# Optimization experiments

Hardware: AMD Instinct MI355X
Metric: run time of the kernel (lower is better)

## Reference

```python
import jax, jax.numpy as jnp
import numpy as np

N_QUBITS = 10
N_LAYERS = 3


def _apply_1q(state, gate, q, batched):
    # state: (B,) + (2,)*n ; gate: (2,2) or (B,2,2)
    s = jnp.moveaxis(state, q + 1, -1)
    shp = s.shape
    s = s.reshape(shp[0], -1, 2)
    eq = 'bij,brj->bri' if batched else 'ij,brj->bri'
    s = jnp.einsum(eq, gate, s).reshape(shp)
    return jnp.moveaxis(s, -1, q + 1)


def _apply_cnot(state, c, t):
    s = jnp.moveaxis(state, (c + 1, t + 1), (-2, -1))
    s = s.at[..., 1, :].set(s[..., 1, ::-1])  # flip target where control==1
    return jnp.moveaxis(s, (-2, -1), (c + 1, t + 1))


def _rot_gate(phi, theta, omega):
    # PennyLane Rot(phi,theta,omega) = RZ(omega) @ RY(theta) @ RZ(phi)
    ch = jnp.cos(theta * 0.5).astype(jnp.complex64)
    sh = jnp.sin(theta * 0.5).astype(jnp.complex64)
    m00 = jnp.exp(-1j * (phi + omega) * 0.5) * ch
    m01 = -jnp.exp(1j * (phi - omega) * 0.5) * sh
    m10 = jnp.exp(-1j * (phi - omega) * 0.5) * sh
    m11 = jnp.exp(1j * (phi + omega) * 0.5) * ch
    return jnp.stack([jnp.stack([m00, m01]), jnp.stack([m10, m11])])


def _circuit(x, weights):
    B = x.shape[0]
    n = N_QUBITS
    state = jnp.zeros((B,) + (2,) * n, jnp.complex64)
    state = state.at[(slice(None),) + (0,) * n].set(1.0)  # |0...0>
    c = jnp.cos(x * 0.5)  # (B, n)
    s = jnp.sin(x * 0.5)
    for l in range(N_LAYERS):
        # AngleEmbedding: RY(x_q) on each wire (batched gates)
        for q in range(n):
            g = jnp.stack([jnp.stack([c[:, q], -s[:, q]], -1),
                           jnp.stack([s[:, q], c[:, q]], -1)], -2).astype(jnp.complex64)
            state = _apply_1q(state, g, q, True)
        # StronglyEntanglingLayers, single sub-layer: Rot on each wire
        for q in range(n):
            g = _rot_gate(weights[l, q, 0], weights[l, q, 1], weights[l, q, 2])
            state = _apply_1q(state, g, q, False)
        # ring of CNOTs with range r=1
        for q in range(n):
            state = _apply_cnot(state, q, (q + 1) % n)
    probs = jnp.abs(state) ** 2  # (B,) + (2,)*n, real
    outs = []
    for q in range(n):
        axes = tuple(a for a in range(1, n + 1) if a != q + 1)
        m = probs.sum(axis=axes)  # (B, 2)
        outs.append(m[:, 0] - m[:, 1])  # <Z_q>
    return jnp.stack(outs, axis=1).astype(jnp.float32)


def setup_inputs() -> dict:
    key = jax.random.key(0)
    k1, k2 = jax.random.split(key)
    x = jax.random.normal(k1, (4096, N_QUBITS), dtype=jnp.float32)
    weights = jax.random.uniform(k2, (N_LAYERS, N_QUBITS, 3), dtype=jnp.float32,
                                 minval=-np.pi, maxval=np.pi)
    return {"x": x, "weights": weights}


def reference(x, weights):
    return _circuit(x, weights)
```

## Files before the change

### kernel.cpp

```cpp
#include <hip/hip_runtime.h>

#define NQ 10
#define NL 3

typedef float v2f __attribute__((ext_vector_type(2)));

__device__ __forceinline__ int   f2i(float v) { union { float f; int i; } u; u.f = v; return u.i; }
__device__ __forceinline__ float i2f(int v)   { union { int i; float f; } u; u.i = v; return u.f; }

__device__ __forceinline__ v2f cmul(v2f a, v2f b) {
    v2f d;
    asm("v_pk_mul_f32 %0, %1, %2 op_sel:[0,0] op_sel_hi:[0,1]"
        : "=v"(d) : "v"(a), "v"(b));
    asm("v_pk_fma_f32 %0, %1, %2, %0 op_sel:[1,1,0] op_sel_hi:[1,0,1] neg_lo:[0,1,0]"
        : "+v"(d) : "v"(a), "v"(b));
    return d;
}

__device__ __forceinline__ v2f pk_ab(v2f A, v2f B, v2f cs) {
    v2f d;
    asm("v_pk_mul_f32 %0, %1, %2 op_sel:[0,1] op_sel_hi:[1,1]"
        : "=v"(d) : "v"(B), "v"(cs));
    asm("v_pk_fma_f32 %0, %1, %2, %0 op_sel:[0,0,0] op_sel_hi:[1,0,1]"
        : "+v"(d) : "v"(A), "v"(cs));
    return d;
}
__device__ __forceinline__ v2f pk_ab_n(v2f A, v2f B, v2f cs) {
    v2f d;
    asm("v_pk_mul_f32 %0, %1, %2 op_sel:[0,1] op_sel_hi:[1,1] neg_lo:[1,0] neg_hi:[1,0]"
        : "=v"(d) : "v"(B), "v"(cs));
    asm("v_pk_fma_f32 %0, %1, %2, %0 op_sel:[0,0,0] op_sel_hi:[1,0,1]"
        : "+v"(d) : "v"(A), "v"(cs));
    return d;
}

template<int C> __device__ __forceinline__ int dppm(int v) {
    return __builtin_amdgcn_mov_dpp(v, C, 0xF, 0xF, false);
}

template<int LM>
__device__ __forceinline__ v2f xlane(v2f v, int baddr) {
    if constexpr (LM == 0) return v;
    int x = f2i(v.x), y = f2i(v.y);
    if constexpr (LM == 1)       { x = dppm<177>(x); y = dppm<177>(y); }
    else if constexpr (LM == 2)  { x = dppm<78>(x);  y = dppm<78>(y); }
    else if constexpr (LM == 3)  { x = dppm<27>(x);  y = dppm<27>(y); }
    else if constexpr (LM < 32) {
        constexpr int off = (LM << 10) | 0x1F;
        x = __builtin_amdgcn_ds_swizzle(x, off);
        y = __builtin_amdgcn_ds_swizzle(y, off);
    } else {
        x = __builtin_amdgcn_ds_bpermute(baddr, x);
        y = __builtin_amdgcn_ds_bpermute(baddr, y);
    }
    return (v2f){ i2f(x), i2f(y) };
}

template<int MASK, int RMASK>
__device__ __forceinline__ void apply_gate(v2f (&a)[16], float4 r0, float4 r1,
                                           float cq, float sq, int lane)
{
    constexpr int LM = (MASK >> 4) & 63;
    constexpr int JM = MASK & 15;
    constexpr int RH = (RMASK >> 4) & 63;
    constexpr int RL = RMASK & 15;

    const v2f vcs = { cq, sq };
    const v2f r0a = { r0.x, r0.y }, r0b = { r0.z, r0.w };
    const v2f r1a = { r1.x, r1.y }, r1b = { r1.z, r1.w };
    const v2f g00 = pk_ab  (r0a, r0b, vcs);
    const v2f g01 = pk_ab_n(r0b, r0a, vcs);
    const v2f g10 = pk_ab  (r1a, r1b, vcs);
    const v2f g11 = pk_ab_n(r1b, r1a, vcs);

    const bool lp = (RH != 0) && (__popc(lane & RH) & 1);
    const v2f A0 = lp ? g11 : g00;
    const v2f B0 = lp ? g10 : g01;
    const v2f A1 = lp ? g00 : g11;
    const v2f B1 = lp ? g01 : g10;

    const int baddr = ((lane ^ LM) << 2);

    v2f o[16];
    #pragma unroll
    for (int j = 0; j < 16; ++j) o[j] = xlane<LM>(a[j ^ JM], baddr);

#define QNN_F(J) { constexpr int SP_ = __builtin_popcount((J) & RL) & 1;      \
    const v2f CA = SP_ ? A1 : A0;                                             \
    const v2f CB = SP_ ? B1 : B0;                                             \
    const v2f av = a[J]; const v2f ov = o[J];                                 \
    v2f d;                                                                    \
    asm("v_pk_mul_f32 %0, %1, %2 op_sel:[0,0] op_sel_hi:[0,1]"                \
        : "=v"(d) : "v"(CA), "v"(av));                    \
    asm("v_pk_fma_f32 %0, %1, %2, %0 op_sel:[1,1,0] op_sel_hi:[1,0,1] neg_lo:[0,1,0]" \
        : "+v"(d) : "v"(CA), "v"(av));                  \
    asm("v_pk_fma_f32 %0, %1, %2, %0 op_sel:[0,0,0] op_sel_hi:[0,1,1]"        \
        : "+v"(d) : "v"(CB), "v"(ov));                  \
    asm("v_pk_fma_f32 %0, %1, %2, %0 op_sel:[1,1,0] op_sel_hi:[1,0,1] neg_lo:[0,1,0]" \
        : "+v"(d) : "v"(CB), "v"(ov));                  \
    a[J] = d; }
    QNN_F(0) QNN_F(1) QNN_F(2) QNN_F(3) QNN_F(4) QNN_F(5) QNN_F(6) QNN_F(7)
    QNN_F(8) QNN_F(9) QNN_F(10) QNN_F(11) QNN_F(12) QNN_F(13) QNN_F(14) QNN_F(15)
#undef QNN_F
}

__global__ __launch_bounds__(256, 4)
void qnn_kernel(const float* __restrict__ x, const float* __restrict__ w,
                float* __restrict__ out)
{
    __shared__ float4 rotL[NL * NQ][2];

    const int t    = threadIdx.x;
    const int lane = t & 63;
    const int b    = blockIdx.x * 4 + (t >> 6);

    if (t < NL * NQ) {
        const float* wp = w + t * 3;
        float phi = wp[0], th = wp[1], om = wp[2];
        float ct = cosf(th * 0.5f), st = sinf(th * 0.5f);
        float ap = (phi + om) * 0.5f, am = (phi - om) * 0.5f;
        float cap = cosf(ap), sap = sinf(ap);
        float cam = cosf(am), sam = sinf(am);
        rotL[t][0] = make_float4(cap * ct, -sap * ct, -cam * st, -sam * st);
        rotL[t][1] = make_float4(cam * st, -sam * st,  cap * ct,  sap * ct);
    }
    __syncthreads();

    const float* xb = x + (size_t)__builtin_amdgcn_readfirstlane(b * NQ);
    float c_[NQ], s_[NQ];
    #pragma unroll
    for (int q = 0; q < NQ; ++q) {
        float xv = xb[q] * 0.5f;
        c_[q] = i2f(__builtin_amdgcn_readfirstlane(f2i(__cosf(xv))));
        s_[q] = i2f(__builtin_amdgcn_readfirstlane(f2i(__sinf(xv))));
    }

    v2f c0[4], c1[4];
    v2f Ln = {1.f, 0.f};
    #pragma unroll
    for (int q = 0; q < NQ; ++q) {
        float4 r0 = rotL[q][0], r1 = rotL[q][1];
        const v2f vcs = { c_[q], s_[q] };
        const v2f r0a = { r0.x, r0.y }, r0b = { r0.z, r0.w };
        const v2f r1a = { r1.x, r1.y }, r1b = { r1.z, r1.w };
        v2f g0 = pk_ab(r0a, r0b, vcs);
        v2f g1 = pk_ab(r1a, r1b, vcs);
        if (q < 4) { c0[q] = g0; c1[q] = g1; }
        else {
            v2f gg = ((lane >> (q - 4)) & 1) ? g1 : g0;
            Ln = (q == 4) ? gg : cmul(Ln, gg);
        }
    }
    v2f S01[4], SH[4];
    #pragma unroll
    for (int j = 0; j < 4; ++j)
        S01[j] = cmul((j & 1) ? c1[0] : c0[0], (j & 2) ? c1[1] : c0[1]);
    #pragma unroll
    for (int h = 0; h < 4; ++h)
        SH[h] = cmul(cmul((h & 1) ? c1[2] : c0[2], (h & 2) ? c1[3] : c0[3]), Ln);
    v2f a[16];
    #pragma unroll
    for (int j = 0; j < 16; ++j)
        a[j] = cmul(S01[j & 3], SH[j >> 2]);

#define GATE(IDX, Q, MASK, RMASK) \
    apply_gate<MASK, RMASK>(a, rotL[IDX][0], rotL[IDX][1], c_[Q], s_[Q], lane);
    GATE(10, 0, 0x003, 0x3FE)  GATE(11, 1, 0x006, 0x003)
    GATE(12, 2, 0x00C, 0x007)  GATE(13, 3, 0x018, 0x00F)
    GATE(14, 4, 0x030, 0x01F)  GATE(15, 5, 0x060, 0x03F)
    GATE(16, 6, 0x0C0, 0x07F)  GATE(17, 7, 0x180, 0x0FF)
    GATE(18, 8, 0x300, 0x1FF)  GATE(19, 9, 0x203, 0x3FF)
    GATE(20, 0, 0x005, 0x2AB)  GATE(21, 1, 0x00A, 0x3FD)
    GATE(22, 2, 0x014, 0x3FA)  GATE(23, 3, 0x028, 0x3F5)
    GATE(24, 4, 0x050, 0x3EA)  GATE(25, 5, 0x0A0, 0x3D5)
    GATE(26, 6, 0x140, 0x3AA)  GATE(27, 7, 0x280, 0x355)
    GATE(28, 8, 0x103, 0x2AA)  GATE(29, 9, 0x206, 0x155)
#undef GATE

    float P[16];
    #pragma unroll
    for (int j = 0; j < 16; ++j)
        P[j] = fmaf(a[j].x, a[j].x, a[j].y * a[j].y);
    #pragma unroll
    for (int bit = 0; bit < 4; ++bit) {
        #pragma unroll
        for (int j = 0; j < 16; ++j)
            if (!(j & (1 << bit))) {
                int k = j | (1 << bit);
                float u = P[j], v = P[k];
                P[j] = u + v;
                P[k] = u - v;
            }
    }

    const int bp32 = ((lane ^ 32) << 2);
    float vout = 0.f;
#define MEAS(Q, RM)                                                           \
    { constexpr int RH_ = ((RM) >> 4) & 63;                                   \
      constexpr int RL_ = (RM) & 15;                                          \
      float v = P[RL_];                                                       \
      if (__popc(lane & RH_) & 1) v = -v;                                     \
      v += i2f(dppm<177>(f2i(v)));                                 \
      v += i2f(dppm<78>(f2i(v)));                                  \
      v += i2f(dppm<321>(dppm<27>(f2i(v))));                  \
      v += i2f(dppm<320>(dppm<321>(f2i(v))));                \
      v += i2f(__builtin_amdgcn_ds_swizzle(f2i(v), (16 << 10) | 0x1F));       \
      v += i2f(__builtin_amdgcn_ds_bpermute(bp32, f2i(v)));                   \
      if (lane == (Q)) vout = v; }
    MEAS(0, 0x0CD) MEAS(1, 0x156) MEAS(2, 0x2AC) MEAS(3, 0x159)
    MEAS(4, 0x2B3) MEAS(5, 0x166) MEAS(6, 0x2CC) MEAS(7, 0x199)
    MEAS(8, 0x333) MEAS(9, 0x266)
#undef MEAS

    if (lane < NQ) out[b * NQ + lane] = vout;
}

extern "C" void kernel_launch(void* const* d_in, const int* in_sizes, int n_in,
                              void* d_out, int out_size, void* d_ws, size_t ws_size,
                              hipStream_t stream) {
    const float* x = (const float*)d_in[0];
    const float* w = (const float*)d_in[1];
    float* out = (float*)d_out;
    const int B = in_sizes[0] / NQ;
    qnn_kernel<<<B / 4, 256, 0, stream>>>(x, w, out);
}
```

Measured before the change: 75.52 us.

## Process two batch samples per wavefront and use permlane swaps for reductions

```diff
diff --git a/kernel.cpp b/kernel.cpp
--- a/kernel.cpp
+++ b/kernel.cpp
@@ -4,6 +4,7 @@
 #define NL 3
 
 typedef float v2f __attribute__((ext_vector_type(2)));
+typedef unsigned int u2 __attribute__((ext_vector_type(2)));
 
 __device__ __forceinline__ int   f2i(float v) { union { float f; int i; } u; u.f = v; return u.i; }
 __device__ __forceinline__ float i2f(int v)   { union { int i; float f; } u; u.i = v; return u.f; }
@@ -36,6 +37,17 @@
 
 template<int C> __device__ __forceinline__ int dppm(int v) {
     return __builtin_amdgcn_mov_dpp(v, C, 0xF, 0xF, false);
+}
+
+__device__ __forceinline__ void pl16_pair(int &x, int &y) {
+    u2 r1 = __builtin_amdgcn_permlane16_swap((unsigned)x, (unsigned)y, false, false);
+    u2 r2 = __builtin_amdgcn_permlane16_swap(r1[1], r1[0], false, false);
+    x = (int)r2[0]; y = (int)r2[1];
+}
+__device__ __forceinline__ void pl32_pair(int &x, int &y) {
+    u2 r1 = __builtin_amdgcn_permlane32_swap((unsigned)x, (unsigned)y, false, false);
+    u2 r2 = __builtin_amdgcn_permlane32_swap(r1[1], r1[0], false, false);
+    x = (int)r2[0]; y = (int)r2[1];
 }
 
 template<int LM>
@@ -57,38 +69,55 @@
 }
 
 template<int MASK, int RMASK>
-__device__ __forceinline__ void apply_gate(v2f (&a)[16], float4 r0, float4 r1,
-                                           float cq, float sq, int lane)
+__device__ __forceinline__ void apply_gate2(v2f (&a0)[16], v2f (&a1)[16],
+                                            float4 r0, float4 r1,
+                                            float cqA, float sqA,
+                                            float cqB, float sqB, int lane)
 {
     constexpr int LM = (MASK >> 4) & 63;
     constexpr int JM = MASK & 15;
     constexpr int RH = (RMASK >> 4) & 63;
     constexpr int RL = RMASK & 15;
 
-    const v2f vcs = { cq, sq };
+    const int baddr = ((lane ^ LM) << 2);
+
+    v2f o0[16];
+    #pragma unroll
+    for (int j = 0; j < 16; ++j) o0[j] = xlane<LM>(a0[j ^ JM], baddr);
+
     const v2f r0a = { r0.x, r0.y }, r0b = { r0.z, r0.w };
     const v2f r1a = { r1.x, r1.y }, r1b = { r1.z, r1.w };
-    const v2f g00 = pk_ab  (r0a, r0b, vcs);
-    const v2f g01 = pk_ab_n(r0b, r0a, vcs);
-    const v2f g10 = pk_ab  (r1a, r1b, vcs);
-    const v2f g11 = pk_ab_n(r1b, r1a, vcs);
-
     const bool lp = (RH != 0) && (__popc(lane & RH) & 1);
-    const v2f A0 = lp ? g11 : g00;
-    const v2f B0 = lp ? g10 : g01;
-    const v2f A1 = lp ? g00 : g11;
-    const v2f B1 = lp ? g01 : g10;
-
-    const int baddr = ((lane ^ LM) << 2);
-
-    v2f o[16];
-    #pragma unroll
-    for (int j = 0; j < 16; ++j) o[j] = xlane<LM>(a[j ^ JM], baddr);
-
-#define QNN_F(J) { constexpr int SP_ = __builtin_popcount((J) & RL) & 1;      \
-    const v2f CA = SP_ ? A1 : A0;                                             \
-    const v2f CB = SP_ ? B1 : B0;                                             \
-    const v2f av = a[J]; const v2f ov = o[J];                                 \
+
+    const v2f vcsA = { cqA, sqA };
+    const v2f g00A = pk_ab  (r0a, r0b, vcsA);
+    const v2f g01A = pk_ab_n(r0b, r0a, vcsA);
+    const v2f g10A = pk_ab  (r1a, r1b, vcsA);
+    const v2f g11A = pk_ab_n(r1b, r1a, vcsA);
+    const v2f A0A = lp ? g11A : g00A;
+    const v2f B0A = lp ? g10A : g01A;
+    const v2f A1A = lp ? g00A : g11A;
+    const v2f B1A = lp ? g01A : g10A;
+
+    const v2f vcsB = { cqB, sqB };
+    const v2f g00B = pk_ab  (r0a, r0b, vcsB);
+    const v2f g01B = pk_ab_n(r0b, r0a, vcsB);
+    const v2f g10B = pk_ab  (r1a, r1b, vcsB);
+    const v2f g11B = pk_ab_n(r1b, r1a, vcsB);
+    const v2f A0B = lp ? g11B : g00B;
+    const v2f B0B = lp ? g10B : g01B;
+    const v2f A1B = lp ? g00B : g11B;
+    const v2f B1B = lp ? g01B : g10B;
+
+    v2f o1[16];
+    #pragma unroll
+    for (int j = 0; j < 16; ++j) o1[j] = xlane<LM>(a1[j ^ JM], baddr);
+
+#define QNN_F(ARR, OARR, A0_, A1_, B0_, B1_, J) {                             \
+    constexpr int SP_ = __builtin_popcount((J) & RL) & 1;                     \
+    const v2f CA = SP_ ? A1_ : A0_;                                           \
+    const v2f CB = SP_ ? B1_ : B0_;                                           \
+    const v2f av = ARR[J]; const v2f ov = OARR[J];                            \
     v2f d;                                                                    \
     asm("v_pk_mul_f32 %0, %1, %2 op_sel:[0,0] op_sel_hi:[0,1]"                \
         : "=v"(d) : "v"(CA), "v"(av));                    \
@@ -98,48 +127,32 @@
         : "+v"(d) : "v"(CB), "v"(ov));                  \
     asm("v_pk_fma_f32 %0, %1, %2, %0 op_sel:[1,1,0] op_sel_hi:[1,0,1] neg_lo:[0,1,0]" \
         : "+v"(d) : "v"(CB), "v"(ov));                  \
-    a[J] = d; }
-    QNN_F(0) QNN_F(1) QNN_F(2) QNN_F(3) QNN_F(4) QNN_F(5) QNN_F(6) QNN_F(7)
-    QNN_F(8) QNN_F(9) QNN_F(10) QNN_F(11) QNN_F(12) QNN_F(13) QNN_F(14) QNN_F(15)
+    ARR[J] = d; }
+#define FMA16(ARR, OARR, A0_, A1_, B0_, B1_)                                  \
+    QNN_F(ARR,OARR,A0_,A1_,B0_,B1_,0)  QNN_F(ARR,OARR,A0_,A1_,B0_,B1_,1)      \
+    QNN_F(ARR,OARR,A0_,A1_,B0_,B1_,2)  QNN_F(ARR,OARR,A0_,A1_,B0_,B1_,3)      \
+    QNN_F(ARR,OARR,A0_,A1_,B0_,B1_,4)  QNN_F(ARR,OARR,A0_,A1_,B0_,B1_,5)      \
+    QNN_F(ARR,OARR,A0_,A1_,B0_,B1_,6)  QNN_F(ARR,OARR,A0_,A1_,B0_,B1_,7)      \
+    QNN_F(ARR,OARR,A0_,A1_,B0_,B1_,8)  QNN_F(ARR,OARR,A0_,A1_,B0_,B1_,9)      \
+    QNN_F(ARR,OARR,A0_,A1_,B0_,B1_,10) QNN_F(ARR,OARR,A0_,A1_,B0_,B1_,11)     \
+    QNN_F(ARR,OARR,A0_,A1_,B0_,B1_,12) QNN_F(ARR,OARR,A0_,A1_,B0_,B1_,13)     \
+    QNN_F(ARR,OARR,A0_,A1_,B0_,B1_,14) QNN_F(ARR,OARR,A0_,A1_,B0_,B1_,15)
+
+    FMA16(a0, o0, A0A, A1A, B0A, B1A)
+    FMA16(a1, o1, A0B, A1B, B0B, B1B)
+#undef FMA16
 #undef QNN_F
 }
 
-__global__ __launch_bounds__(256, 4)
-void qnn_kernel(const float* __restrict__ x, const float* __restrict__ w,
-                float* __restrict__ out)
+__device__ __forceinline__ void layer1(v2f (&a)[16], const float (&c_)[NQ],
+                                       const float (&s_)[NQ],
+                                       const float4 (*rot)[2], int lane)
 {
-    __shared__ float4 rotL[NL * NQ][2];
-
-    const int t    = threadIdx.x;
-    const int lane = t & 63;
-    const int b    = blockIdx.x * 4 + (t >> 6);
-
-    if (t < NL * NQ) {
-        const float* wp = w + t * 3;
-        float phi = wp[0], th = wp[1], om = wp[2];
-        float ct = cosf(th * 0.5f), st = sinf(th * 0.5f);
-        float ap = (phi + om) * 0.5f, am = (phi - om) * 0.5f;
-        float cap = cosf(ap), sap = sinf(ap);
-        float cam = cosf(am), sam = sinf(am);
-        rotL[t][0] = make_float4(cap * ct, -sap * ct, -cam * st, -sam * st);
-        rotL[t][1] = make_float4(cam * st, -sam * st,  cap * ct,  sap * ct);
-    }
-    __syncthreads();
-
-    const float* xb = x + (size_t)__builtin_amdgcn_readfirstlane(b * NQ);
-    float c_[NQ], s_[NQ];
-    #pragma unroll
-    for (int q = 0; q < NQ; ++q) {
-        float xv = xb[q] * 0.5f;
-        c_[q] = i2f(__builtin_amdgcn_readfirstlane(f2i(__cosf(xv))));
-        s_[q] = i2f(__builtin_amdgcn_readfirstlane(f2i(__sinf(xv))));
-    }
-
     v2f c0[4], c1[4];
     v2f Ln = {1.f, 0.f};
     #pragma unroll
     for (int q = 0; q < NQ; ++q) {
-        float4 r0 = rotL[q][0], r1 = rotL[q][1];
+        float4 r0 = rot[q][0], r1 = rot[q][1];
         const v2f vcs = { c_[q], s_[q] };
         const v2f r0a = { r0.x, r0.y }, r0b = { r0.z, r0.w };
         const v2f r1a = { r1.x, r1.y }, r1b = { r1.z, r1.w };
@@ -158,13 +171,52 @@
     #pragma unroll
     for (int h = 0; h < 4; ++h)
         SH[h] = cmul(cmul((h & 1) ? c1[2] : c0[2], (h & 2) ? c1[3] : c0[3]), Ln);
-    v2f a[16];
     #pragma unroll
     for (int j = 0; j < 16; ++j)
         a[j] = cmul(S01[j & 3], SH[j >> 2]);
-
-#define GATE(IDX, Q, MASK, RMASK) \
-    apply_gate<MASK, RMASK>(a, rotL[IDX][0], rotL[IDX][1], c_[Q], s_[Q], lane);
+}
+
+__global__ __launch_bounds__(256, 2)
+void qnn_kernel(const float* __restrict__ x, const float* __restrict__ w,
+                float* __restrict__ out)
+{
+    __shared__ float4 rotL[NL * NQ][2];
+
+    const int t    = threadIdx.x;
+    const int lane = t & 63;
+    const int wv   = blockIdx.x * 4 + (t >> 6);
+
+    if (t < NL * NQ) {
+        const float* wp = w + t * 3;
+        float phi = wp[0], th = wp[1], om = wp[2];
+        float ct = cosf(th * 0.5f), st = sinf(th * 0.5f);
+        float ap = (phi + om) * 0.5f, am = (phi - om) * 0.5f;
+        float cap = cosf(ap), sap = sinf(ap);
+        float cam = cosf(am), sam = sinf(am);
+        rotL[t][0] = make_float4(cap * ct, -sap * ct, -cam * st, -sam * st);
+        rotL[t][1] = make_float4(cam * st, -sam * st,  cap * ct,  sap * ct);
+    }
+    __syncthreads();
+
+    const float* xb = x + (size_t)__builtin_amdgcn_readfirstlane(wv * 2 * NQ);
+    float cA[NQ], sA[NQ], cB[NQ], sB[NQ];
+    #pragma unroll
+    for (int q = 0; q < NQ; ++q) {
+        float xv = xb[q] * 0.5f;
+        cA[q] = i2f(__builtin_amdgcn_readfirstlane(f2i(__cosf(xv))));
+        sA[q] = i2f(__builtin_amdgcn_readfirstlane(f2i(__sinf(xv))));
+        float xw = xb[NQ + q] * 0.5f;
+        cB[q] = i2f(__builtin_amdgcn_readfirstlane(f2i(__cosf(xw))));
+        sB[q] = i2f(__builtin_amdgcn_readfirstlane(f2i(__sinf(xw))));
+    }
+
+    v2f a0[16], a1[16];
+    layer1(a0, cA, sA, rotL, lane);
+    layer1(a1, cB, sB, rotL, lane);
+
+#define GATE(IDX, Q, MASK, RMASK)                                             \
+    apply_gate2<MASK, RMASK>(a0, a1, rotL[IDX][0], rotL[IDX][1],              \
+                             cA[Q], sA[Q], cB[Q], sB[Q], lane);
     GATE(10, 0, 0x003, 0x3FE)  GATE(11, 1, 0x006, 0x003)
     GATE(12, 2, 0x00C, 0x007)  GATE(13, 3, 0x018, 0x00F)
     GATE(14, 4, 0x030, 0x01F)  GATE(15, 5, 0x060, 0x03F)
@@ -177,42 +229,56 @@
     GATE(28, 8, 0x103, 0x2AA)  GATE(29, 9, 0x206, 0x155)
 #undef GATE
 
-    float P[16];
+    v2f P[16];
     #pragma unroll
     for (int j = 0; j < 16; ++j)
-        P[j] = fmaf(a[j].x, a[j].x, a[j].y * a[j].y);
+        P[j] = (v2f){ fmaf(a0[j].x, a0[j].x, a0[j].y * a0[j].y),
+                      fmaf(a1[j].x, a1[j].x, a1[j].y * a1[j].y) };
     #pragma unroll
     for (int bit = 0; bit < 4; ++bit) {
         #pragma unroll
         for (int j = 0; j < 16; ++j)
             if (!(j & (1 << bit))) {
                 int k = j | (1 << bit);
-                float u = P[j], v = P[k];
+                v2f u = P[j], v = P[k];
                 P[j] = u + v;
                 P[k] = u - v;
             }
     }
 
-    const int bp32 = ((lane ^ 32) << 2);
-    float vout = 0.f;
+    v2f vout = {0.f, 0.f};
 #define MEAS(Q, RM)                                                           \
     { constexpr int RH_ = ((RM) >> 4) & 63;                                   \
       constexpr int RL_ = (RM) & 15;                                          \
-      float v = P[RL_];                                                       \
+      v2f v = P[RL_];                                                         \
       if (__popc(lane & RH_) & 1) v = -v;                                     \
-      v += i2f(dppm<177>(f2i(v)));                                 \
-      v += i2f(dppm<78>(f2i(v)));                                  \
-      v += i2f(dppm<321>(dppm<27>(f2i(v))));                  \
-      v += i2f(dppm<320>(dppm<321>(f2i(v))));                \
-      v += i2f(__builtin_amdgcn_ds_swizzle(f2i(v), (16 << 10) | 0x1F));       \
-      v += i2f(__builtin_amdgcn_ds_bpermute(bp32, f2i(v)));                   \
+      v2f tt;                                                                 \
+      tt.x = i2f(dppm<177>(f2i(v.x))); tt.y = i2f(dppm<177>(f2i(v.y)));       \
+      v += tt;                                                     \
+      tt.x = i2f(dppm<78>(f2i(v.x)));  tt.y = i2f(dppm<78>(f2i(v.y)));        \
+      v += tt;                                                     \
+      tt.x = i2f(dppm<321>(dppm<27>(f2i(v.x))));                              \
+      tt.y = i2f(dppm<321>(dppm<27>(f2i(v.y))));                              \
+      v += tt;                                                \
+      tt.x = i2f(dppm<320>(dppm<321>(f2i(v.x))));                             \
+      tt.y = i2f(dppm<320>(dppm<321>(f2i(v.y))));                             \
+      v += tt;                                               \
+      { int px = f2i(v.x), py = f2i(v.y); pl16_pair(px, py);                  \
+        tt = (v2f){ i2f(px), i2f(py) }; }                                     \
+      v += tt;                                        \
+      { int px = f2i(v.x), py = f2i(v.y); pl32_pair(px, py);                  \
+        tt = (v2f){ i2f(px), i2f(py) }; }                                     \
+      v += tt;                                        \
       if (lane == (Q)) vout = v; }
     MEAS(0, 0x0CD) MEAS(1, 0x156) MEAS(2, 0x2AC) MEAS(3, 0x159)
     MEAS(4, 0x2B3) MEAS(5, 0x166) MEAS(6, 0x2CC) MEAS(7, 0x199)
     MEAS(8, 0x333) MEAS(9, 0x266)
 #undef MEAS
 
-    if (lane < NQ) out[b * NQ + lane] = vout;
+    if (lane < NQ) {
+        out[(wv * 2)     * NQ + lane] = vout.x;
+        out[(wv * 2 + 1) * NQ + lane] = vout.y;
+    }
 }
 
 extern "C" void kernel_launch(void* const* d_in, const int* in_sizes, int n_in,
@@ -222,5 +288,5 @@
     const float* w = (const float*)d_in[1];
     float* out = (float*)d_out;
     const int B = in_sizes[0] / NQ;
-    qnn_kernel<<<B / 4, 256, 0, stream>>>(x, w, out);
-}
+    qnn_kernel<<<B / 8, 256, 0, stream>>>(x, w, out);
+}
```

New measurement: 77.35 us. 1.02x slower.

## Split each state vector across two wavefronts with LDS exchange for bit-3 gates

Applied to the files above, without the earlier changes.

```diff
diff --git a/kernel.cpp b/kernel.cpp
--- a/kernel.cpp
+++ b/kernel.cpp
@@ -7,6 +7,9 @@
 
 __device__ __forceinline__ int   f2i(float v) { union { float f; int i; } u; u.f = v; return u.i; }
 __device__ __forceinline__ float i2f(int v)   { union { int i; float f; } u; u.i = v; return u.f; }
+__device__ __forceinline__ float uf(float v) {
+    return i2f(__builtin_amdgcn_readfirstlane(f2i(v)));
+}
 
 __device__ __forceinline__ v2f cmul(v2f a, v2f b) {
     v2f d;
@@ -16,7 +19,6 @@
         : "+v"(d) : "v"(a), "v"(b));
     return d;
 }
-
 __device__ __forceinline__ v2f pk_ab(v2f A, v2f B, v2f cs) {
     v2f d;
     asm("v_pk_mul_f32 %0, %1, %2 op_sel:[0,1] op_sel_hi:[1,1]"
@@ -56,14 +58,32 @@
     return (v2f){ i2f(x), i2f(y) };
 }
 
-template<int MASK, int RMASK>
-__device__ __forceinline__ void apply_gate(v2f (&a)[16], float4 r0, float4 r1,
-                                           float cq, float sq, int lane)
+template<int MASK, int RMASK, bool CROSS>
+__device__ __forceinline__ void agate(v2f (&a)[8], float4 r0, float4 r1,
+                                      float cq, float sq, int lane, int wid,
+                                      v2f (*xch)[8][64])
 {
-    constexpr int LM = (MASK >> 4) & 63;
-    constexpr int JM = MASK & 15;
-    constexpr int RH = (RMASK >> 4) & 63;
-    constexpr int RL = RMASK & 15;
+    constexpr int LM  = (MASK >> 4) & 63;
+    constexpr int JM  = MASK & 15;
+    constexpr int JML = JM & 7;
+    constexpr int RH  = (RMASK >> 4) & 63;
+    constexpr int RL  = RMASK & 15;
+    constexpr int RL3 = (RL >> 3) & 1;
+    constexpr int RLL = RL & 7;
+
+    v2f o[8];
+    if constexpr (!CROSS) {
+        const int baddr = ((lane ^ LM) << 2);
+        #pragma unroll
+        for (int j = 0; j < 8; ++j) o[j] = xlane<LM>(a[j ^ JML], baddr);
+    } else {
+        #pragma unroll
+        for (int j = 0; j < 8; ++j) xch[wid][j][lane] = a[j];
+        __syncthreads();
+        #pragma unroll
+        for (int j = 0; j < 8; ++j) o[j] = xch[wid ^ 1][j ^ JML][lane ^ LM];
+        __syncthreads();
+    }
 
     const v2f vcs = { cq, sq };
     const v2f r0a = { r0.x, r0.y }, r0b = { r0.z, r0.w };
@@ -73,19 +93,14 @@
     const v2f g10 = pk_ab  (r1a, r1b, vcs);
     const v2f g11 = pk_ab_n(r1b, r1a, vcs);
 
-    const bool lp = (RH != 0) && (__popc(lane & RH) & 1);
-    const v2f A0 = lp ? g11 : g00;
-    const v2f B0 = lp ? g10 : g01;
-    const v2f A1 = lp ? g00 : g11;
-    const v2f B1 = lp ? g01 : g10;
-
-    const int baddr = ((lane ^ LM) << 2);
-
-    v2f o[16];
-    #pragma unroll
-    for (int j = 0; j < 16; ++j) o[j] = xlane<LM>(a[j ^ JM], baddr);
-
-#define QNN_F(J) { constexpr int SP_ = __builtin_popcount((J) & RL) & 1;      \
+    const bool lp0 = (RH != 0) && (__popc(lane & RH) & 1);
+    const bool lpw = lp0 != ((RL3 != 0) && (wid != 0));
+    const v2f A0 = lpw ? g11 : g00;
+    const v2f B0 = lpw ? g10 : g01;
+    const v2f A1 = lpw ? g00 : g11;
+    const v2f B1 = lpw ? g01 : g10;
+
+#define QNN_F(J) { constexpr int SP_ = __builtin_popcount((J) & RLL) & 1;     \
     const v2f CA = SP_ ? A1 : A0;                                             \
     const v2f CB = SP_ ? B1 : B0;                                             \
     const v2f av = a[J]; const v2f ov = o[J];                                 \
@@ -100,19 +115,20 @@
         : "+v"(d) : "v"(CB), "v"(ov));                  \
     a[J] = d; }
     QNN_F(0) QNN_F(1) QNN_F(2) QNN_F(3) QNN_F(4) QNN_F(5) QNN_F(6) QNN_F(7)
-    QNN_F(8) QNN_F(9) QNN_F(10) QNN_F(11) QNN_F(12) QNN_F(13) QNN_F(14) QNN_F(15)
 #undef QNN_F
 }
 
-__global__ __launch_bounds__(256, 4)
+__global__ __launch_bounds__(128, 8)
 void qnn_kernel(const float* __restrict__ x, const float* __restrict__ w,
                 float* __restrict__ out)
 {
     __shared__ float4 rotL[NL * NQ][2];
+    __shared__ v2f    xch[2][8][64];
 
     const int t    = threadIdx.x;
     const int lane = t & 63;
-    const int b    = blockIdx.x * 4 + (t >> 6);
+    const int wid  = t >> 6;
+    const int b    = blockIdx.x;
 
     if (t < NL * NQ) {
         const float* wp = w + t * 3;
@@ -126,13 +142,13 @@
     }
     __syncthreads();
 
-    const float* xb = x + (size_t)__builtin_amdgcn_readfirstlane(b * NQ);
+    const float* xb = x + (size_t)b * NQ;
     float c_[NQ], s_[NQ];
     #pragma unroll
     for (int q = 0; q < NQ; ++q) {
         float xv = xb[q] * 0.5f;
-        c_[q] = i2f(__builtin_amdgcn_readfirstlane(f2i(__cosf(xv))));
-        s_[q] = i2f(__builtin_amdgcn_readfirstlane(f2i(__sinf(xv))));
+        c_[q] = uf(__cosf(xv));
+        s_[q] = uf(__sinf(xv));
     }
 
     v2f c0[4], c1[4];
@@ -158,13 +174,14 @@
     #pragma unroll
     for (int h = 0; h < 4; ++h)
         SH[h] = cmul(cmul((h & 1) ? c1[2] : c0[2], (h & 2) ? c1[3] : c0[3]), Ln);
-    v2f a[16];
-    #pragma unroll
-    for (int j = 0; j < 16; ++j)
-        a[j] = cmul(S01[j & 3], SH[j >> 2]);
-
-#define GATE(IDX, Q, MASK, RMASK) \
-    apply_gate<MASK, RMASK>(a, rotL[IDX][0], rotL[IDX][1], c_[Q], s_[Q], lane);
+    v2f a[8];
+    #pragma unroll
+    for (int j = 0; j < 8; ++j)
+        a[j] = cmul(S01[j & 3], SH[(wid << 1) | (j >> 2)]);
+
+#define GATE(IDX, Q, MASK, RMASK)                                             \
+    agate<MASK, RMASK, ((MASK & 8) != 0)>(a, rotL[IDX][0], rotL[IDX][1],      \
+                                          c_[Q], s_[Q], lane, wid, xch);
     GATE(10, 0, 0x003, 0x3FE)  GATE(11, 1, 0x006, 0x003)
     GATE(12, 2, 0x00C, 0x007)  GATE(13, 3, 0x018, 0x00F)
     GATE(14, 4, 0x030, 0x01F)  GATE(15, 5, 0x060, 0x03F)
@@ -177,14 +194,14 @@
     GATE(28, 8, 0x103, 0x2AA)  GATE(29, 9, 0x206, 0x155)
 #undef GATE
 
-    float P[16];
-    #pragma unroll
-    for (int j = 0; j < 16; ++j)
+    float P[8];
+    #pragma unroll
+    for (int j = 0; j < 8; ++j)
         P[j] = fmaf(a[j].x, a[j].x, a[j].y * a[j].y);
     #pragma unroll
-    for (int bit = 0; bit < 4; ++bit) {
-        #pragma unroll
-        for (int j = 0; j < 16; ++j)
+    for (int bit = 0; bit < 3; ++bit) {
+        #pragma unroll
+        for (int j = 0; j < 8; ++j)
             if (!(j & (1 << bit))) {
                 int k = j | (1 << bit);
                 float u = P[j], v = P[k];
@@ -192,13 +209,20 @@
                 P[k] = u - v;
             }
     }
+    #pragma unroll
+    for (int j = 0; j < 8; ++j) xch[wid][j][lane].x = P[j];
+    __syncthreads();
+    #pragma unroll
+    for (int j = 0; j < 8; ++j) {
+        float po = xch[wid ^ 1][j][lane].x;
+        P[j] = (wid == 0) ? (P[j] + po) : (po - P[j]);
+    }
 
     const int bp32 = ((lane ^ 32) << 2);
-    float vout = 0.f;
 #define MEAS(Q, RM)                                                           \
     { constexpr int RH_ = ((RM) >> 4) & 63;                                   \
       constexpr int RL_ = (RM) & 15;                                          \
-      float v = P[RL_];                                                       \
+      float v = P[RL_ & 7];                                                   \
       if (__popc(lane & RH_) & 1) v = -v;                                     \
       v += i2f(dppm<177>(f2i(v)));                                 \
       v += i2f(dppm<78>(f2i(v)));                                  \
@@ -206,13 +230,11 @@
       v += i2f(dppm<320>(dppm<321>(f2i(v))));                \
       v += i2f(__builtin_amdgcn_ds_swizzle(f2i(v), (16 << 10) | 0x1F));       \
       v += i2f(__builtin_amdgcn_ds_bpermute(bp32, f2i(v)));                   \
-      if (lane == (Q)) vout = v; }
+      if (wid == (RL_ >> 3) && lane == (Q)) out[b * NQ + (Q)] = v; }
     MEAS(0, 0x0CD) MEAS(1, 0x156) MEAS(2, 0x2AC) MEAS(3, 0x159)
     MEAS(4, 0x2B3) MEAS(5, 0x166) MEAS(6, 0x2CC) MEAS(7, 0x199)
     MEAS(8, 0x333) MEAS(9, 0x266)
 #undef MEAS
-
-    if (lane < NQ) out[b * NQ + lane] = vout;
 }
 
 extern "C" void kernel_launch(void* const* d_in, const int* in_sizes, int n_in,
@@ -222,5 +244,5 @@
     const float* w = (const float*)d_in[1];
     float* out = (float*)d_out;
     const int B = in_sizes[0] / NQ;
-    qnn_kernel<<<B / 4, 256, 0, stream>>>(x, w, out);
-}
+    qnn_kernel<<<B, 128, 0, stream>>>(x, w, out);
+}
```

Result: slower. 86.85 us (+15.0%).
